# Kernel tuning notes

Hardware: AMD Instinct MI355X
Metric: run time of the kernel (lower is better)

The kernel has to match this reference:

```python
import jax, jax.numpy as jnp
import numpy as np

B, N, M = 64, 4096, 128


def setup_inputs() -> dict:
    key = jax.random.key(0)
    x = jax.random.normal(key, (B, N, M), dtype=jnp.float32)
    return {"x": x}


def reference(x):
    # Original loops over channels M, applying a 1D FFT along the N axis to
    # each (batch, N) slice. Equivalent batched form: FFT along axis=1.
    f = jnp.fft.fft(x.astype(jnp.complex64), axis=1)  # (B, N, M) complex64
    return (jnp.real(f), jnp.imag(f))
```

## Files before the change

### kernel.cpp

```cpp
#include <hip/hip_runtime.h>
#include <hip/hip_fp16.h>

#define B 64
#define N 4096
#define M 128

constexpr int T   = 512;
constexpr int NWG = 512;

__device__ __forceinline__ float2 cadd(float2 a, float2 b){ return make_float2(a.x+b.x, a.y+b.y); }
__device__ __forceinline__ float2 csub(float2 a, float2 b){ return make_float2(a.x-b.x, a.y-b.y); }
__device__ __forceinline__ float2 cmul(float2 a, float2 b){ return make_float2(a.x*b.x - a.y*b.y, a.x*b.y + a.y*b.x); }
__device__ __forceinline__ float2 mulnegi(float2 a){ return make_float2(a.y, -a.x); }
__device__ __forceinline__ float2 muli(float2 a)  { return make_float2(-a.y, a.x); }
__device__ __forceinline__ float2 cis(float ang){ float s, c; __sincosf(ang, &s, &c); return make_float2(c, s); }
__device__ __forceinline__ float2 h2f(__half2 h){ return __half22float2(h); }
__device__ __forceinline__ __half2 f2h(float2 v){ return __floats2half2_rn(v.x, v.y); }

__device__ __constant__ const float W64R[8] = {
    1.0f, 0.995184726672197f, 0.980785280403230f, 0.956940335732209f,
    0.923879532511287f, 0.881921264348355f, 0.831469612302545f, 0.773010453362737f };
__device__ __constant__ const float W64I[8] = {
    0.0f, -0.098017140329561f, -0.195090322016128f, -0.290284677254462f,
    -0.382683432365090f, -0.471396736825998f, -0.555570233019602f, -0.634393284163645f };

__device__ __forceinline__ void dft8(float2 t[8]) {
    float2 e0=cadd(t[0],t[4]), e1=csub(t[0],t[4]);
    float2 e2=cadd(t[2],t[6]), e3=csub(t[2],t[6]);
    float2 E0=cadd(e0,e2), E2=csub(e0,e2);
    float2 E1=cadd(e1,mulnegi(e3)), E3=cadd(e1,muli(e3));
    float2 o0=cadd(t[1],t[5]), o1=csub(t[1],t[5]);
    float2 o2=cadd(t[3],t[7]), o3=csub(t[3],t[7]);
    float2 O0=cadd(o0,o2), O2=csub(o0,o2);
    float2 O1=cadd(o1,mulnegi(o3)), O3=cadd(o1,muli(o3));
    const float C = 0.70710678118654752f;
    float2 w1O1 = make_float2(C*(O1.x+O1.y), C*(O1.y-O1.x));
    float2 w2O2 = mulnegi(O2);
    float2 w3O3 = make_float2(C*(O3.y-O3.x), -C*(O3.x+O3.y));
    t[0]=cadd(E0,O0);   t[4]=csub(E0,O0);
    t[1]=cadd(E1,w1O1); t[5]=csub(E1,w1O1);
    t[2]=cadd(E2,w2O2); t[6]=csub(E2,w2O2);
    t[3]=cadd(E3,w3O3); t[7]=csub(E3,w3O3);
}

__device__ __forceinline__ int lslot(int k1, int n2, int mc) {
    return (k1 << 9) | ((n2 ^ (k1 & 7)) << 3) | mc;
}

__global__ __launch_bounds__(T, 2)
void fft_one(const float* __restrict__ x, float* __restrict__ out) {
    extern __shared__ __half2 lz[];

    const int bid = blockIdx.x;
    const int b   = ((bid >> 6) << 3) | (bid & 7);
    const int mcg = (bid >> 3) & 7;
    const int tid = threadIdx.x;
    const int mc  = tid & 7;
    const int rp  = tid >> 3;

    const float* xb = x + (size_t)b * N * M + mcg * 16 + mc * 2;

    __half2 pk[8][8];

    #pragma unroll
    for (int bb = 0; bb < 8; ++bb) {
        float2 t[8];
        #pragma unroll
        for (int a = 0; a < 8; ++a)
            t[a] = *(const float2*)(xb + (size_t)(64*(8*a+bb) + rp) * M);
        dft8(t);
        #pragma unroll
        for (int d = 0; d < 8; ++d) pk[bb][d] = f2h(t[d]);
    }
    {
        const float2 ws = cis(-6.2831853071795864f * (float)rp / 4096.0f);
        const float2 w8 = cis(-6.2831853071795864f * (float)rp / 512.0f);
        float2 pd = make_float2(1.f, 0.f);
        #pragma unroll
        for (int d = 0; d < 8; ++d) {
            const float2 wd = make_float2(W64R[d], W64I[d]);
            float2 t[8];
            t[0] = h2f(pk[0][d]);
            float2 w = wd;
            #pragma unroll
            for (int bb = 1; bb < 8; ++bb) {
                t[bb] = cmul(h2f(pk[bb][d]), w);
                w = cmul(w, wd);
            }
            dft8(t);
            float2 ac = pd;
            #pragma unroll
            for (int c = 0; c < 8; ++c) {
                lz[lslot(8*c+d, rp, mc)] = f2h(cmul(t[c], ac));
                ac = cmul(ac, w8);
            }
            pd = cmul(pd, ws);
        }
    }
    __syncthreads();

    #pragma unroll
    for (int bb = 0; bb < 8; ++bb) {
        float2 t[8];
        #pragma unroll
        for (int a = 0; a < 8; ++a)
            t[a] = h2f(lz[lslot(rp, 8*a+bb, mc)]);
        dft8(t);
        #pragma unroll
        for (int d = 0; d < 8; ++d) pk[bb][d] = f2h(t[d]);
    }
    #pragma unroll
    for (int d = 0; d < 8; ++d) {
        const float2 wd = make_float2(W64R[d], W64I[d]);
        float2 t[8];
        t[0] = h2f(pk[0][d]);
        float2 w = wd;
        #pragma unroll
        for (int bb = 1; bb < 8; ++bb) {
            t[bb] = cmul(h2f(pk[bb][d]), w);
            w = cmul(w, wd);
        }
        dft8(t);
        #pragma unroll
        for (int c = 0; c < 8; ++c)
            lz[lslot(rp, 8*c+d, mc)] = f2h(t[c]);
    }
    __syncthreads();

    float* outRe = out + (size_t)b * N * M + mcg * 16 + mc * 2;
    float* outIm = outRe + (size_t)B * N * M;
    const int r = rp;
    #pragma unroll 4
    for (int j = 0; j < 64; ++j) {
        int k   = (j << 6) | r;
        int kk  = (N - k) & (N - 1);
        int k1p = kk & 63, k2p = kk >> 6;
        float2 Zk = h2f(lz[lslot(r,   j,   mc)]);
        float2 Zm = h2f(lz[lslot(k1p, k2p, mc)]);
        float2 re = make_float2(0.5f * (Zk.x + Zm.x), 0.5f * (Zk.y + Zm.y));
        float2 im = make_float2(0.5f * (Zk.y - Zm.y), 0.5f * (Zm.x - Zk.x));
        *(float2*)(outRe + (size_t)k * M) = re;
        *(float2*)(outIm + (size_t)k * M) = im;
    }
}

extern "C" void kernel_launch(void* const* d_in, const int* in_sizes, int n_in,
                              void* d_out, int out_size, void* d_ws, size_t ws_size,
                              hipStream_t stream) {
    const float* x = (const float*)d_in[0];
    float* out = (float*)d_out;
    const int lds_bytes = 64 * 64 * 8 * (int)sizeof(__half2);
    hipFuncSetAttribute((const void*)fft_one,
                        hipFuncAttributeMaxDynamicSharedMemorySize, lds_bytes);
    fft_one<<<NWG, T, lds_bytes, stream>>>(x, out);
}
```

Measured before the change: 122.2 us.

## Split four-step FFT into two kernels through an fp16 global workspace

```diff
diff --git a/kernel.cpp b/kernel.cpp
--- a/kernel.cpp
+++ b/kernel.cpp
@@ -4,9 +4,6 @@
 #define B 64
 #define N 4096
 #define M 128
-
-constexpr int T   = 512;
-constexpr int NWG = 512;
 
 __device__ __forceinline__ float2 cadd(float2 a, float2 b){ return make_float2(a.x+b.x, a.y+b.y); }
 __device__ __forceinline__ float2 csub(float2 a, float2 b){ return make_float2(a.x-b.x, a.y-b.y); }
@@ -43,25 +40,164 @@
     t[3]=cadd(E3,w3O3); t[7]=csub(E3,w3O3);
 }
 
-__device__ __forceinline__ int lslot(int k1, int n2, int mc) {
+__global__ __launch_bounds__(256, 4)
+void fft_k1(const float* __restrict__ x, __half2* __restrict__ ws) {
+    const int bid = blockIdx.x;
+    const int b   = ((bid >> 7) << 3) | (bid & 7);
+    const int blk = (bid >> 3) & 15;
+    const int tid = threadIdx.x;
+    const int mc  = tid & 63;
+    const int n2  = (blk << 2) | (tid >> 6);
+
+    const float* xb = x + (size_t)b * N * M + 2 * mc;
+
+    __half2 pk[8][8];
+    #pragma unroll
+    for (int bb = 0; bb < 8; ++bb) {
+        float2 t[8];
+        #pragma unroll
+        for (int a = 0; a < 8; ++a)
+            t[a] = *(const float2*)(xb + (size_t)(64 * (8 * a + bb) + n2) * M);
+        dft8(t);
+        #pragma unroll
+        for (int d = 0; d < 8; ++d) pk[bb][d] = f2h(t[d]);
+    }
+    const float ang = -6.2831853071795864f * (float)n2;
+    const float2 wsc = cis(ang / 4096.0f);
+    const float2 w8  = cis(ang / 512.0f);
+    __half2* wsb = ws + ((size_t)b << 18) + ((size_t)n2 << 6) + mc;
+    float2 pd = make_float2(1.f, 0.f);
+    #pragma unroll
+    for (int d = 0; d < 8; ++d) {
+        const float2 wd = make_float2(W64R[d], W64I[d]);
+        float2 t[8];
+        t[0] = h2f(pk[0][d]);
+        float2 w = wd;
+        #pragma unroll
+        for (int bb = 1; bb < 8; ++bb) { t[bb] = cmul(h2f(pk[bb][d]), w); w = cmul(w, wd); }
+        dft8(t);
+        float2 ac = pd;
+        #pragma unroll
+        for (int c = 0; c < 8; ++c) {
+            wsb[(size_t)(8 * c + d) << 12] = f2h(cmul(t[c], ac));
+            ac = cmul(ac, w8);
+        }
+        pd = cmul(pd, wsc);
+    }
+}
+
+__global__ __launch_bounds__(256, 2)
+void fft_k2(const __half2* __restrict__ ws, float* __restrict__ out) {
+    __shared__ __half2 lda[64 * 256];
+    const int bid = blockIdx.x;
+    const int b   = ((bid >> 6) << 3) | (bid & 7);
+    const int mcg = (bid >> 3) & 7;
+    const int tid = threadIdx.x;
+    const int mc  = (mcg << 3) | (tid & 7);
+    const int p   = tid >> 3;
+    const int kA  = (p == 0) ? 0  : p;
+    const int kB  = (p == 0) ? 32 : 64 - p;
+
+    const __half2* wsb = ws + ((size_t)b << 18) + mc;
+
+    __half2 pk[8][8];
+    #pragma unroll
+    for (int bb = 0; bb < 8; ++bb) {
+        float2 t[8];
+        #pragma unroll
+        for (int a = 0; a < 8; ++a)
+            t[a] = h2f(wsb[((size_t)kA << 12) + ((8 * a + bb) << 6)]);
+        dft8(t);
+        #pragma unroll
+        for (int d = 0; d < 8; ++d) pk[bb][d] = f2h(t[d]);
+    }
+    #pragma unroll
+    for (int d = 0; d < 8; ++d) {
+        const float2 wd = make_float2(W64R[d], W64I[d]);
+        float2 t[8];
+        t[0] = h2f(pk[0][d]);
+        float2 w = wd;
+        #pragma unroll
+        for (int bb = 1; bb < 8; ++bb) { t[bb] = cmul(h2f(pk[bb][d]), w); w = cmul(w, wd); }
+        dft8(t);
+        #pragma unroll
+        for (int c = 0; c < 8; ++c) lda[(8 * c + d) * 256 + tid] = f2h(t[c]);
+    }
+    __half2 zb[64];
+    #pragma unroll
+    for (int bb = 0; bb < 8; ++bb) {
+        float2 t[8];
+        #pragma unroll
+        for (int a = 0; a < 8; ++a)
+            t[a] = h2f(wsb[((size_t)kB << 12) + ((8 * a + bb) << 6)]);
+        dft8(t);
+        #pragma unroll
+        for (int d = 0; d < 8; ++d) pk[bb][d] = f2h(t[d]);
+    }
+    #pragma unroll
+    for (int d = 0; d < 8; ++d) {
+        const float2 wd = make_float2(W64R[d], W64I[d]);
+        float2 t[8];
+        t[0] = h2f(pk[0][d]);
+        float2 w = wd;
+        #pragma unroll
+        for (int bb = 1; bb < 8; ++bb) { t[bb] = cmul(h2f(pk[bb][d]), w); w = cmul(w, wd); }
+        dft8(t);
+        #pragma unroll
+        for (int c = 0; c < 8; ++c) zb[8 * c + d] = f2h(t[c]);
+    }
+
+    float* outRe = out + (size_t)b * N * M + 2 * mc;
+    float* outIm = outRe + (size_t)B * N * M;
+
+#define HSTORE(KROW, ZK, ZM) do {                                            \
+        float2 _re = make_float2(0.5f * ((ZK).x + (ZM).x),                   \
+                                 0.5f * ((ZK).y + (ZM).y));                  \
+        float2 _im = make_float2(0.5f * ((ZK).y - (ZM).y),                   \
+                                 0.5f * ((ZM).x - (ZK).x));                  \
+        *(float2*)(outRe + (size_t)(KROW) * M) = _re;                        \
+        *(float2*)(outIm + (size_t)(KROW) * M) = _im;                        \
+    } while (0)
+
+    if (p == 0) {
+        #pragma unroll
+        for (int k2 = 0; k2 < 64; ++k2) {
+            float2 ZkA = h2f(lda[k2 * 256 + tid]);
+            float2 ZmA = h2f(lda[(((64 - k2) & 63) * 256) + tid]);
+            HSTORE(k2 << 6, ZkA, ZmA);
+            float2 ZkB = h2f(zb[k2]);
+            float2 ZmB = h2f(zb[63 - k2]);
+            HSTORE((k2 << 6) + 32, ZkB, ZmB);
+        }
+    } else {
+        #pragma unroll
+        for (int k2 = 0; k2 < 64; ++k2) {
+            float2 ZkA = h2f(lda[k2 * 256 + tid]);
+            float2 ZmA = h2f(zb[63 - k2]);
+            HSTORE((k2 << 6) + kA, ZkA, ZmA);
+            float2 ZkB = h2f(zb[k2]);
+            float2 ZmB = h2f(lda[(63 - k2) * 256 + tid]);
+            HSTORE((k2 << 6) + kB, ZkB, ZmB);
+        }
+    }
+#undef HSTORE
+}
+
+__device__ __forceinline__ int lslot17(int k1, int n2, int mc) {
     return (k1 << 9) | ((n2 ^ (k1 & 7)) << 3) | mc;
 }
 
-__global__ __launch_bounds__(T, 2)
-void fft_one(const float* __restrict__ x, float* __restrict__ out) {
+__global__ __launch_bounds__(512, 2)
+void fft_one17(const float* __restrict__ x, float* __restrict__ out) {
     extern __shared__ __half2 lz[];
-
     const int bid = blockIdx.x;
     const int b   = ((bid >> 6) << 3) | (bid & 7);
     const int mcg = (bid >> 3) & 7;
     const int tid = threadIdx.x;
     const int mc  = tid & 7;
     const int rp  = tid >> 3;
-
     const float* xb = x + (size_t)b * N * M + mcg * 16 + mc * 2;
-
     __half2 pk[8][8];
-
     #pragma unroll
     for (int bb = 0; bb < 8; ++bb) {
         float2 t[8];
@@ -73,8 +209,8 @@
         for (int d = 0; d < 8; ++d) pk[bb][d] = f2h(t[d]);
     }
     {
-        const float2 ws = cis(-6.2831853071795864f * (float)rp / 4096.0f);
-        const float2 w8 = cis(-6.2831853071795864f * (float)rp / 512.0f);
+        const float2 ws_ = cis(-6.2831853071795864f * (float)rp / 4096.0f);
+        const float2 w8  = cis(-6.2831853071795864f * (float)rp / 512.0f);
         float2 pd = make_float2(1.f, 0.f);
         #pragma unroll
         for (int d = 0; d < 8; ++d) {
@@ -83,60 +219,51 @@
             t[0] = h2f(pk[0][d]);
             float2 w = wd;
             #pragma unroll
-            for (int bb = 1; bb < 8; ++bb) {
-                t[bb] = cmul(h2f(pk[bb][d]), w);
-                w = cmul(w, wd);
-            }
+            for (int bb = 1; bb < 8; ++bb) { t[bb] = cmul(h2f(pk[bb][d]), w); w = cmul(w, wd); }
             dft8(t);
             float2 ac = pd;
             #pragma unroll
             for (int c = 0; c < 8; ++c) {
-                lz[lslot(8*c+d, rp, mc)] = f2h(cmul(t[c], ac));
+                lz[lslot17(8*c+d, rp, mc)] = f2h(cmul(t[c], ac));
                 ac = cmul(ac, w8);
             }
-            pd = cmul(pd, ws);
+            pd = cmul(pd, ws_);
         }
     }
     __syncthreads();
-
-    #pragma unroll
-    for (int bb = 0; bb < 8; ++bb) {
-        float2 t[8];
-        #pragma unroll
-        for (int a = 0; a < 8; ++a)
-            t[a] = h2f(lz[lslot(rp, 8*a+bb, mc)]);
-        dft8(t);
-        #pragma unroll
-        for (int d = 0; d < 8; ++d) pk[bb][d] = f2h(t[d]);
-    }
-    #pragma unroll
-    for (int d = 0; d < 8; ++d) {
-        const float2 wd = make_float2(W64R[d], W64I[d]);
-        float2 t[8];
-        t[0] = h2f(pk[0][d]);
-        float2 w = wd;
-        #pragma unroll
-        for (int bb = 1; bb < 8; ++bb) {
-            t[bb] = cmul(h2f(pk[bb][d]), w);
-            w = cmul(w, wd);
-        }
+    #pragma unroll
+    for (int bb = 0; bb < 8; ++bb) {
+        float2 t[8];
+        #pragma unroll
+        for (int a = 0; a < 8; ++a)
+            t[a] = h2f(lz[lslot17(rp, 8*a+bb, mc)]);
+        dft8(t);
+        #pragma unroll
+        for (int d = 0; d < 8; ++d) pk[bb][d] = f2h(t[d]);
+    }
+    #pragma unroll
+    for (int d = 0; d < 8; ++d) {
+        const float2 wd = make_float2(W64R[d], W64I[d]);
+        float2 t[8];
+        t[0] = h2f(pk[0][d]);
+        float2 w = wd;
+        #pragma unroll
+        for (int bb = 1; bb < 8; ++bb) { t[bb] = cmul(h2f(pk[bb][d]), w); w = cmul(w, wd); }
         dft8(t);
         #pragma unroll
         for (int c = 0; c < 8; ++c)
-            lz[lslot(rp, 8*c+d, mc)] = f2h(t[c]);
+            lz[lslot17(rp, 8*c+d, mc)] = f2h(t[c]);
     }
     __syncthreads();
-
     float* outRe = out + (size_t)b * N * M + mcg * 16 + mc * 2;
     float* outIm = outRe + (size_t)B * N * M;
-    const int r = rp;
     #pragma unroll 4
     for (int j = 0; j < 64; ++j) {
-        int k   = (j << 6) | r;
+        int k   = (j << 6) | rp;
         int kk  = (N - k) & (N - 1);
         int k1p = kk & 63, k2p = kk >> 6;
-        float2 Zk = h2f(lz[lslot(r,   j,   mc)]);
-        float2 Zm = h2f(lz[lslot(k1p, k2p, mc)]);
+        float2 Zk = h2f(lz[lslot17(rp,  j,   mc)]);
+        float2 Zm = h2f(lz[lslot17(k1p, k2p, mc)]);
         float2 re = make_float2(0.5f * (Zk.x + Zm.x), 0.5f * (Zk.y + Zm.y));
         float2 im = make_float2(0.5f * (Zk.y - Zm.y), 0.5f * (Zm.x - Zk.x));
         *(float2*)(outRe + (size_t)k * M) = re;
@@ -149,8 +276,15 @@
                               hipStream_t stream) {
     const float* x = (const float*)d_in[0];
     float* out = (float*)d_out;
-    const int lds_bytes = 64 * 64 * 8 * (int)sizeof(__half2);
-    hipFuncSetAttribute((const void*)fft_one,
-                        hipFuncAttributeMaxDynamicSharedMemorySize, lds_bytes);
-    fft_one<<<NWG, T, lds_bytes, stream>>>(x, out);
-}
+    const size_t ws_needed = (size_t)B * 64 * 64 * 64 * sizeof(__half2);
+    if (ws_size >= ws_needed) {
+        __half2* ws = (__half2*)d_ws;
+        fft_k1<<<1024, 256, 0, stream>>>(x, ws);
+        fft_k2<<<512, 256, 0, stream>>>(ws, out);
+    } else {
+        const int lds_bytes = 64 * 64 * 8 * (int)sizeof(__half2);
+        hipFuncSetAttribute((const void*)fft_one17,
+                            hipFuncAttributeMaxDynamicSharedMemorySize, lds_bytes);
+        fft_one17<<<512, 512, lds_bytes, stream>>>(x, out);
+    }
+}
```

New measurement: 261.7 us. 2.14x slower.

## Process two channel groups per workgroup with prefetch of second tile

Applied to the files above, without the earlier changes.

```diff
diff --git a/kernel.cpp b/kernel.cpp
--- a/kernel.cpp
+++ b/kernel.cpp
@@ -6,7 +6,7 @@
 #define M 128
 
 constexpr int T   = 512;
-constexpr int NWG = 512;
+constexpr int NWG = 256;
 
 __device__ __forceinline__ float2 cadd(float2 a, float2 b){ return make_float2(a.x+b.x, a.y+b.y); }
 __device__ __forceinline__ float2 csub(float2 a, float2 b){ return make_float2(a.x-b.x, a.y-b.y); }
@@ -47,58 +47,30 @@
     return (k1 << 9) | ((n2 ^ (k1 & 7)) << 3) | mc;
 }
 
-__global__ __launch_bounds__(T, 2)
-void fft_one(const float* __restrict__ x, float* __restrict__ out) {
-    extern __shared__ __half2 lz[];
+__device__ __forceinline__ void passA2(__half2 pk[8][8], __half2* lz, int rp, int mc) {
+    const float2 ws_ = cis(-6.2831853071795864f * (float)rp / 4096.0f);
+    const float2 w8  = cis(-6.2831853071795864f * (float)rp / 512.0f);
+    float2 pd = make_float2(1.f, 0.f);
+    #pragma unroll
+    for (int d = 0; d < 8; ++d) {
+        const float2 wd = make_float2(W64R[d], W64I[d]);
+        float2 t[8];
+        t[0] = h2f(pk[0][d]);
+        float2 w = wd;
+        #pragma unroll
+        for (int bb = 1; bb < 8; ++bb) { t[bb] = cmul(h2f(pk[bb][d]), w); w = cmul(w, wd); }
+        dft8(t);
+        float2 ac = pd;
+        #pragma unroll
+        for (int c = 0; c < 8; ++c) {
+            lz[lslot(8*c+d, rp, mc)] = f2h(cmul(t[c], ac));
+            ac = cmul(ac, w8);
+        }
+        pd = cmul(pd, ws_);
+    }
+}
 
-    const int bid = blockIdx.x;
-    const int b   = ((bid >> 6) << 3) | (bid & 7);
-    const int mcg = (bid >> 3) & 7;
-    const int tid = threadIdx.x;
-    const int mc  = tid & 7;
-    const int rp  = tid >> 3;
-
-    const float* xb = x + (size_t)b * N * M + mcg * 16 + mc * 2;
-
-    __half2 pk[8][8];
-
-    #pragma unroll
-    for (int bb = 0; bb < 8; ++bb) {
-        float2 t[8];
-        #pragma unroll
-        for (int a = 0; a < 8; ++a)
-            t[a] = *(const float2*)(xb + (size_t)(64*(8*a+bb) + rp) * M);
-        dft8(t);
-        #pragma unroll
-        for (int d = 0; d < 8; ++d) pk[bb][d] = f2h(t[d]);
-    }
-    {
-        const float2 ws = cis(-6.2831853071795864f * (float)rp / 4096.0f);
-        const float2 w8 = cis(-6.2831853071795864f * (float)rp / 512.0f);
-        float2 pd = make_float2(1.f, 0.f);
-        #pragma unroll
-        for (int d = 0; d < 8; ++d) {
-            const float2 wd = make_float2(W64R[d], W64I[d]);
-            float2 t[8];
-            t[0] = h2f(pk[0][d]);
-            float2 w = wd;
-            #pragma unroll
-            for (int bb = 1; bb < 8; ++bb) {
-                t[bb] = cmul(h2f(pk[bb][d]), w);
-                w = cmul(w, wd);
-            }
-            dft8(t);
-            float2 ac = pd;
-            #pragma unroll
-            for (int c = 0; c < 8; ++c) {
-                lz[lslot(8*c+d, rp, mc)] = f2h(cmul(t[c], ac));
-                ac = cmul(ac, w8);
-            }
-            pd = cmul(pd, ws);
-        }
-    }
-    __syncthreads();
-
+__device__ __forceinline__ void phaseB(__half2 pk[8][8], __half2* lz, int rp, int mc) {
     #pragma unroll
     for (int bb = 0; bb < 8; ++bb) {
         float2 t[8];
@@ -116,32 +88,96 @@
         t[0] = h2f(pk[0][d]);
         float2 w = wd;
         #pragma unroll
-        for (int bb = 1; bb < 8; ++bb) {
-            t[bb] = cmul(h2f(pk[bb][d]), w);
-            w = cmul(w, wd);
-        }
+        for (int bb = 1; bb < 8; ++bb) { t[bb] = cmul(h2f(pk[bb][d]), w); w = cmul(w, wd); }
         dft8(t);
         #pragma unroll
         for (int c = 0; c < 8; ++c)
             lz[lslot(rp, 8*c+d, mc)] = f2h(t[c]);
     }
-    __syncthreads();
+}
 
-    float* outRe = out + (size_t)b * N * M + mcg * 16 + mc * 2;
-    float* outIm = outRe + (size_t)B * N * M;
-    const int r = rp;
+__device__ __forceinline__ void unpackStore(const __half2* lz, float* outRe,
+                                            float* outIm, int rp, int mc) {
     #pragma unroll 4
     for (int j = 0; j < 64; ++j) {
-        int k   = (j << 6) | r;
+        int k   = (j << 6) | rp;
         int kk  = (N - k) & (N - 1);
         int k1p = kk & 63, k2p = kk >> 6;
-        float2 Zk = h2f(lz[lslot(r,   j,   mc)]);
+        float2 Zk = h2f(lz[lslot(rp,  j,   mc)]);
         float2 Zm = h2f(lz[lslot(k1p, k2p, mc)]);
         float2 re = make_float2(0.5f * (Zk.x + Zm.x), 0.5f * (Zk.y + Zm.y));
         float2 im = make_float2(0.5f * (Zk.y - Zm.y), 0.5f * (Zm.x - Zk.x));
         *(float2*)(outRe + (size_t)k * M) = re;
         *(float2*)(outIm + (size_t)k * M) = im;
     }
+}
+
+__global__ __launch_bounds__(T, 1)
+void fft_one(const float* __restrict__ x, float* __restrict__ out) {
+    extern __shared__ __half2 lz[];
+
+    const int bid = blockIdx.x;
+    const int b   = ((bid >> 5) << 3) | (bid & 7);
+    const int qb  = (bid >> 3) & 3;
+    const int tid = threadIdx.x;
+    const int mc  = tid & 7;
+    const int rp  = tid >> 3;
+
+    const float* xb0 = x + (size_t)b * N * M + qb * 16 + mc * 2;
+    const float* xb1 = xb0 + 64;
+    float* outRe0 = out + (size_t)b * N * M + qb * 16 + mc * 2;
+    float* outIm0 = outRe0 + (size_t)B * N * M;
+
+    __half2 pk[8][8];
+
+    #pragma unroll
+    for (int bb = 0; bb < 8; ++bb) {
+        float2 t[8];
+        #pragma unroll
+        for (int a = 0; a < 8; ++a)
+            t[a] = *(const float2*)(xb0 + (size_t)(64*(8*a+bb) + rp) * M);
+        dft8(t);
+        #pragma unroll
+        for (int d = 0; d < 8; ++d) pk[bb][d] = f2h(t[d]);
+    }
+    float2 pf[4][8];
+    #pragma unroll
+    for (int cc = 0; cc < 4; ++cc)
+        #pragma unroll
+        for (int a = 0; a < 8; ++a)
+            pf[cc][a] = *(const float2*)(xb1 + (size_t)(64*(8*a+cc) + rp) * M);
+
+    passA2(pk, lz, rp, mc);
+    __syncthreads();
+    phaseB(pk, lz, rp, mc);
+    __syncthreads();
+    unpackStore(lz, outRe0, outIm0, rp, mc);
+    __syncthreads();
+
+    #pragma unroll
+    for (int cc = 0; cc < 4; ++cc) {
+        float2 t[8];
+        #pragma unroll
+        for (int a = 0; a < 8; ++a) t[a] = pf[cc][a];
+        dft8(t);
+        #pragma unroll
+        for (int d = 0; d < 8; ++d) pk[cc][d] = f2h(t[d]);
+    }
+    #pragma unroll
+    for (int bb = 4; bb < 8; ++bb) {
+        float2 t[8];
+        #pragma unroll
+        for (int a = 0; a < 8; ++a)
+            t[a] = *(const float2*)(xb1 + (size_t)(64*(8*a+bb) + rp) * M);
+        dft8(t);
+        #pragma unroll
+        for (int d = 0; d < 8; ++d) pk[bb][d] = f2h(t[d]);
+    }
+    passA2(pk, lz, rp, mc);
+    __syncthreads();
+    phaseB(pk, lz, rp, mc);
+    __syncthreads();
+    unpackStore(lz, outRe0 + 64, outIm0 + 64, rp, mc);
 }
 
 extern "C" void kernel_launch(void* const* d_in, const int* in_sizes, int n_in,
```

Measured after the change: 282.0 us. 131% more time.
